# Kernel tuning notes

Measured on AMD Instinct MI355X. Metric: run time of the kernel, lower is better.

## Reference

```python
import jax, jax.numpy as jnp
import numpy as np

B, T, V, D, C, O = 64, 128, 32, 128, 10000, 512


def setup_inputs() -> dict:
    key = jax.random.key(0)
    ks = jax.random.split(key, 14)
    s = 1.0 / np.sqrt(D)
    # ragged visit sequences: codes in [1, C), padded visits are all-zero codes
    codes = jax.random.randint(ks[0], (B, T, V), 1, C, dtype=jnp.int32)
    lengths = jax.random.randint(ks[1], (B,), 1, T + 1, dtype=jnp.int32)
    visit_mask = (jnp.arange(T)[None, :] < lengths[:, None])
    codes_x = codes * visit_mask[:, :, None].astype(jnp.int32)
    emb = (jax.random.normal(ks[2], (C, D), jnp.float32) * 0.02).at[0].set(0.0)
    return {
        "codes_x": codes_x,
        "emb": emb,
        "a_kernel": jax.random.normal(ks[3], (D, 3 * D), jnp.float32) * s,
        "a_rec": jax.random.normal(ks[4], (D, 3 * D), jnp.float32) * s,
        "a_bias": jnp.zeros((2, 3 * D), jnp.float32),
        "b_kernel": jax.random.normal(ks[5], (D, 3 * D), jnp.float32) * s,
        "b_rec": jax.random.normal(ks[6], (D, 3 * D), jnp.float32) * s,
        "b_bias": jnp.zeros((2, 3 * D), jnp.float32),
        "alpha_w": jax.random.normal(ks[7], (D, 1), jnp.float32) * s,
        "alpha_b": jnp.zeros((1,), jnp.float32),
        "beta_w": jax.random.normal(ks[8], (D, D), jnp.float32) * s,
        "beta_b": jnp.zeros((D,), jnp.float32),
        "cls_w": jax.random.normal(ks[9], (D, O), jnp.float32) * s,
        "cls_b": jnp.zeros((O,), jnp.float32),
    }


def gru(x, mask, kernel, rec, bias):
    """Keras GRU (reset_after=True), masked: carries state+output through padded steps.
    x: [B,T,D], mask: [B,T] bool -> [B,T,D]."""
    bi, br = bias[0], bias[1]
    xp = x @ kernel + bi  # [B,T,3D] precomputed input projection

    def step(h, inp):
        xp_t, m_t = inp
        hp = h @ rec + br
        xz, xr, xh = jnp.split(xp_t, 3, axis=-1)
        hz, hr, hh = jnp.split(hp, 3, axis=-1)
        z = jax.nn.sigmoid(xz + hz)
        r = jax.nn.sigmoid(xr + hr)
        hcand = jnp.tanh(xh + r * hh)
        h_new = z * h + (1.0 - z) * hcand
        h_out = jnp.where(m_t[:, None], h_new, h)
        return h_out, h_out

    h0 = jnp.zeros((x.shape[0], rec.shape[0]), x.dtype)
    _, ys = jax.lax.scan(step, h0, (jnp.swapaxes(xp, 0, 1), jnp.swapaxes(mask, 0, 1)))
    return jnp.swapaxes(ys, 0, 1)


def retain_forward(codes_x, emb, a_kernel, a_rec, a_bias, b_kernel, b_rec, b_bias,
                   alpha_w, alpha_b, beta_w, beta_b, cls_w, cls_b):
    x = emb[codes_x].sum(axis=2)                     # [B,T,D] visit embeddings
    mask = x.sum(axis=-1) != 0                       # [B,T] visit mask
    lengths = mask.sum(axis=-1)                      # [B]
    # masked reverse: rx[b, j] = x[b, lengths[b]-1-j] for j < lengths[b], else 0
    t = x.shape[1]
    idx = lengths[:, None] - 1 - jnp.arange(t)[None, :]  # [B,T]
    valid = idx >= 0
    rx = jnp.take_along_axis(x, jnp.clip(idx, 0, t - 1)[:, :, None], axis=1)
    rx = rx * valid[:, :, None].astype(x.dtype)
    # dual GRU attention (dropout inactive at inference)
    g = gru(rx, mask, a_kernel, a_rec, a_bias)
    h = gru(rx, mask, b_kernel, b_rec, b_bias)
    attn_alpha = jax.nn.softmax(g @ alpha_w + alpha_b, axis=1)   # [B,T,1]
    attn_beta = jnp.tanh(h @ beta_w + beta_b)                    # [B,T,D]
    c = jnp.sum(attn_alpha * attn_beta * x, axis=1)              # [B,D]
    return c @ cls_w + cls_b                                     # [B,O]


def reference(codes_x, emb, a_kernel, a_rec, a_bias, b_kernel, b_rec, b_bias,
              alpha_w, alpha_b, beta_w, beta_b, cls_w, cls_b):
    return retain_forward(codes_x, emb, a_kernel, a_rec, a_bias, b_kernel, b_rec,
                          b_bias, alpha_w, alpha_b, beta_w, beta_b, cls_w, cls_b)
```

## Files before the change

kernel.cpp:

```cpp
#include <hip/hip_runtime.h>
#include <math.h>

#define BATCH 64
#define TT 128
#define VV 32
#define DD 128
#define OO 512
#define N3 384
#define NN 768

#define OFF_X      0u
#define OFF_XPC    1048576u
#define OFF_GSEQ   7340032u
#define OFF_HSEQ   8388608u
#define OFF_INTS   9437184u
#define OFF_ALPHA  9453632u
#define OFF_CPART  9461824u

__global__ __launch_bounds__(128) void k_gather(const int* __restrict__ codes,
        const float* __restrict__ emb, float* __restrict__ x, int* __restrict__ mask) {
    int bt = blockIdx.x;
    int d = threadIdx.x;
    const int* cp = codes + (size_t)bt * VV;
    float acc = 0.f;
    #pragma unroll 8
    for (int v = 0; v < VV; ++v) {
        int code = cp[v];
        acc += emb[(size_t)code * DD + d];
    }
    x[(size_t)bt * DD + d] = acc;
    float s = acc;
    #pragma unroll
    for (int off = 32; off; off >>= 1) s += __shfl_xor(s, off);
    __shared__ float red[2];
    if ((d & 63) == 0) red[d >> 6] = s;
    __syncthreads();
    if (d == 0) mask[bt] = ((red[0] + red[1]) != 0.0f) ? 1 : 0;
}

__global__ __launch_bounds__(128) void k_len(const int* __restrict__ mask,
        int* __restrict__ lengths, int* __restrict__ ridx) {
    int b = blockIdx.x, t = threadIdx.x;
    int m = mask[b * TT + t];
    unsigned long long bal = __ballot(m != 0);
    __shared__ int cnt[2];
    if ((t & 63) == 0) cnt[t >> 6] = __popcll(bal);
    __syncthreads();
    int len = cnt[0] + cnt[1];
    if (t == 0) lengths[b] = len;
    ridx[b * TT + t] = len - 1 - t;
}

__global__ __launch_bounds__(256) void k_xp(const float* __restrict__ x,
        const float* __restrict__ akern, const float* __restrict__ bkern,
        const float* __restrict__ abias, const float* __restrict__ bbias,
        float* __restrict__ xpc) {
    __shared__ __attribute__((aligned(16))) float As[32][68];
    __shared__ __attribute__((aligned(16))) float Bs[32][68];
    int mb = blockIdx.x, nb = blockIdx.y;
    int n0 = nb * 64;
    int tid = threadIdx.x;
    int tx = tid & 15, ty = tid >> 4;
    float acc[4][4] = {};
    for (int k0 = 0; k0 < DD; k0 += 32) {
        #pragma unroll
        for (int i = 0; i < 2; ++i) {
            int s = tid * 2 + i;
            int row = s >> 3, kk = (s & 7) * 4;
            float4 v = *reinterpret_cast<const float4*>(x + (size_t)(mb * 64 + row) * DD + k0 + kk);
            As[kk][row] = v.x; As[kk+1][row] = v.y; As[kk+2][row] = v.z; As[kk+3][row] = v.w;
        }
        #pragma unroll
        for (int i = 0; i < 2; ++i) {
            int s = tid * 2 + i;
            int kk = s >> 4, c = (s & 15) * 4;
            int n = n0 + c;
            const float* src = (n < N3) ? (akern + (size_t)(k0 + kk) * N3 + n)
                                        : (bkern + (size_t)(k0 + kk) * N3 + (n - N3));
            *reinterpret_cast<float4*>(&Bs[kk][c]) = *reinterpret_cast<const float4*>(src);
        }
        __syncthreads();
        #pragma unroll
        for (int kk = 0; kk < 32; ++kk) {
            float4 a = *reinterpret_cast<const float4*>(&As[kk][ty * 4]);
            float4 bv = *reinterpret_cast<const float4*>(&Bs[kk][tx * 4]);
            float av[4] = {a.x, a.y, a.z, a.w};
            float bw[4] = {bv.x, bv.y, bv.z, bv.w};
            #pragma unroll
            for (int i2 = 0; i2 < 4; ++i2)
                #pragma unroll
                for (int j2 = 0; j2 < 4; ++j2)
                    acc[i2][j2] = fmaf(av[i2], bw[j2], acc[i2][j2]);
        }
        __syncthreads();
    }
    int nbase = n0 + tx * 4;
    float4 bias;
    if (nbase < N3) bias = *reinterpret_cast<const float4*>(abias + nbase);
    else            bias = *reinterpret_cast<const float4*>(bbias + (nbase - N3));
    #pragma unroll
    for (int i2 = 0; i2 < 4; ++i2) {
        int m = mb * 64 + ty * 4 + i2;
        float4 o;
        o.x = acc[i2][0] + bias.x; o.y = acc[i2][1] + bias.y;
        o.z = acc[i2][2] + bias.z; o.w = acc[i2][3] + bias.w;
        *reinterpret_cast<float4*>(xpc + (size_t)m * NN + nbase) = o;
    }
}

__device__ __forceinline__ float fast_sigmoid(float x) {
    return 1.f / (1.f + __expf(-x));
}
__device__ __forceinline__ float fast_tanh(float x) {
    float xc = fminf(fmaxf(x, -15.f), 15.f);
    float e2 = __expf(2.f * xc);
    return (e2 - 1.f) / (e2 + 1.f);
}

#define LOADW(i) \
    float4 w##i = *reinterpret_cast<const float4*>(rec + (size_t)(krow0 + i) * N3 + j4); \
    asm volatile("" : "+v"(w##i.x), "+v"(w##i.y), "+v"(w##i.z), "+v"(w##i.w));
#define DOTQ(q, i0, i1, i2, i3) { \
    float4 hv = *reinterpret_cast<const float4*>(&h_lds[krow0 + 4 * (q)]); \
    acc.x = fmaf(hv.x, w##i0.x, acc.x); acc.y = fmaf(hv.x, w##i0.y, acc.y); \
    acc.z = fmaf(hv.x, w##i0.z, acc.z); acc.w = fmaf(hv.x, w##i0.w, acc.w); \
    acc.x = fmaf(hv.y, w##i1.x, acc.x); acc.y = fmaf(hv.y, w##i1.y, acc.y); \
    acc.z = fmaf(hv.y, w##i1.z, acc.z); acc.w = fmaf(hv.y, w##i1.w, acc.w); \
    acc.x = fmaf(hv.z, w##i2.x, acc.x); acc.y = fmaf(hv.z, w##i2.y, acc.y); \
    acc.z = fmaf(hv.z, w##i2.z, acc.z); acc.w = fmaf(hv.z, w##i2.w, acc.w); \
    acc.x = fmaf(hv.w, w##i3.x, acc.x); acc.y = fmaf(hv.w, w##i3.y, acc.y); \
    acc.z = fmaf(hv.w, w##i3.z, acc.z); acc.w = fmaf(hv.w, w##i3.w, acc.w); }

__global__ __launch_bounds__(768, 3)
void k_gru(
        const float* __restrict__ arec, const float* __restrict__ abias,
        const float* __restrict__ brec, const float* __restrict__ bbias,
        const float* __restrict__ xpc, const int* __restrict__ mask,
        const int* __restrict__ ridx, float* __restrict__ gseq, float* __restrict__ hseq) {
    int b = blockIdx.x & 63;
    int gru = blockIdx.x >> 6;
    const float* rec  = gru ? brec : arec;
    const float* bias = gru ? bbias : abias;
    float* seq = gru ? hseq : gseq;
    int t = threadIdx.x;
    int c4 = t % 96;
    int kc = t / 96;
    int j4 = c4 * 4;
    int krow0 = kc * 16;
    LOADW(0)  LOADW(1)  LOADW(2)  LOADW(3)
    LOADW(4)  LOADW(5)  LOADW(6)  LOADW(7)
    LOADW(8)  LOADW(9)  LOADW(10) LOADW(11)
    LOADW(12) LOADW(13) LOADW(14) LOADW(15)
    __shared__ __attribute__((aligned(16))) float h_lds[DD];
    __shared__ __attribute__((aligned(16))) float part[8 * N3];
    __shared__ int smask[TT];
    __shared__ int sridx[TT];
    if (t < TT) { smask[t] = mask[b * TT + t]; sridx[t] = ridx[b * TT + t]; }
    if (t < DD) h_lds[t] = 0.f;
    float bz_r = 0.f, br_r = 0.f, bh_r = 0.f, bz_i = 0.f, br_i = 0.f, bh_i = 0.f;
    if (t < DD) {
        bz_r = bias[N3 + t];  br_r = bias[N3 + DD + t];  bh_r = bias[N3 + 2 * DD + t];
        bz_i = bias[t];       br_i = bias[DD + t];       bh_i = bias[2 * DD + t];
    }
    float hreg = 0.f;
    __syncthreads();
    const float* xpb = xpc + (size_t)b * TT * NN + gru * N3;
    for (int step = 0; step < TT; ++step) {
        int m = smask[step];
        if (!m) {
            if (t < DD) seq[(size_t)(b * TT + step) * DD + t] = hreg;
            continue;
        }
        float xz = 0.f, xr = 0.f, xh = 0.f;
        if (t < DD) {
            int row = sridx[step];
            if (row >= 0) {
                const float* xrow = xpb + (size_t)row * NN;
                xz = xrow[t]; xr = xrow[DD + t]; xh = xrow[2 * DD + t];
            } else {
                xz = bz_i; xr = br_i; xh = bh_i;
            }
        }
        float4 acc = {0.f, 0.f, 0.f, 0.f};
        DOTQ(0, 0, 1, 2, 3)
        DOTQ(1, 4, 5, 6, 7)
        DOTQ(2, 8, 9, 10, 11)
        DOTQ(3, 12, 13, 14, 15)
        *reinterpret_cast<float4*>(&part[kc * N3 + j4]) = acc;
        __syncthreads();
        if (t < DD) {
            float hz = bz_r, hr = br_r, hh = bh_r;
            #pragma unroll
            for (int g = 0; g < 8; ++g) {
                hz += part[g * N3 + t];
                hr += part[g * N3 + DD + t];
                hh += part[g * N3 + 2 * DD + t];
            }
            float z = fast_sigmoid(xz + hz);
            float r = fast_sigmoid(xr + hr);
            float hc = fast_tanh(xh + r * hh);
            float hnew = z * hreg + (1.f - z) * hc;
            hreg = hnew;
            h_lds[t] = hnew;
            seq[(size_t)(b * TT + step) * DD + t] = hnew;
        }
        __syncthreads();
    }
}

__global__ __launch_bounds__(128) void k_alpha(const float* __restrict__ gseq,
        const float* __restrict__ alpha_w, const float* __restrict__ alpha_b,
        float* __restrict__ alpha) {
    int b = blockIdx.x, t = threadIdx.x;
    __shared__ float aw[DD];
    aw[t] = alpha_w[t];
    __syncthreads();
    const float* g = gseq + (size_t)(b * TT + t) * DD;
    float acc = 0.f;
    #pragma unroll
    for (int k = 0; k < DD; k += 4) {
        float4 gv = *reinterpret_cast<const float4*>(g + k);
        acc = fmaf(gv.x, aw[k],     acc);
        acc = fmaf(gv.y, aw[k + 1], acc);
        acc = fmaf(gv.z, aw[k + 2], acc);
        acc = fmaf(gv.w, aw[k + 3], acc);
    }
    float logit = acc + alpha_b[0];
    float mx = logit;
    #pragma unroll
    for (int off = 32; off; off >>= 1) mx = fmaxf(mx, __shfl_xor(mx, off));
    __shared__ float redm[2];
    if ((t & 63) == 0) redm[t >> 6] = mx;
    __syncthreads();
    mx = fmaxf(redm[0], redm[1]);
    float e = expf(logit - mx);
    float s = e;
    #pragma unroll
    for (int off = 32; off; off >>= 1) s += __shfl_xor(s, off);
    __shared__ float reds[2];
    if ((t & 63) == 0) reds[t >> 6] = s;
    __syncthreads();
    alpha[b * TT + t] = e / (reds[0] + reds[1]);
}

__global__ __launch_bounds__(128) void k_beta(const float* __restrict__ hseq,
        const float* __restrict__ x, const float* __restrict__ beta_w,
        const float* __restrict__ beta_b, const float* __restrict__ alpha,
        float* __restrict__ cpart) {
    __shared__ __attribute__((aligned(16))) float bw[DD][DD];
    __shared__ __attribute__((aligned(16))) float hr[4][DD];
    __shared__ float cred[4][DD];
    int b = blockIdx.x >> 3, grp = blockIdx.x & 7;
    int tid = threadIdx.x;
    for (int i = tid; i < DD * DD / 4; i += 128) {
        float4 v = *reinterpret_cast<const float4*>(beta_w + (size_t)i * 4);
        *reinterpret_cast<float4*>(&bw[0][0] + (size_t)i * 4) = v;
    }
    int trow = tid >> 5, dq = (tid & 31) * 4;
    float bb0 = beta_b[dq], bb1 = beta_b[dq + 1], bb2 = beta_b[dq + 2], bb3 = beta_b[dq + 3];
    float c0 = 0.f, c1 = 0.f, c2 = 0.f, c3 = 0.f;
    for (int tg = 0; tg < 4; ++tg) {
        int t = grp * 16 + tg * 4 + trow;
        size_t rowoff = (size_t)(b * TT + t) * DD;
        float4 hv = *reinterpret_cast<const float4*>(hseq + rowoff + dq);
        __syncthreads();
        *reinterpret_cast<float4*>(&hr[trow][dq]) = hv;
        __syncthreads();
        float a0 = 0.f, a1 = 0.f, a2 = 0.f, a3 = 0.f;
        #pragma unroll 8
        for (int k = 0; k < DD; ++k) {
            float hk = hr[trow][k];
            float4 w = *reinterpret_cast<const float4*>(&bw[k][dq]);
            a0 = fmaf(hk, w.x, a0); a1 = fmaf(hk, w.y, a1);
            a2 = fmaf(hk, w.z, a2); a3 = fmaf(hk, w.w, a3);
        }
        float al = alpha[b * TT + t];
        float4 xv = *reinterpret_cast<const float4*>(x + rowoff + dq);
        c0 = fmaf(al * tanhf(a0 + bb0), xv.x, c0);
        c1 = fmaf(al * tanhf(a1 + bb1), xv.y, c1);
        c2 = fmaf(al * tanhf(a2 + bb2), xv.z, c2);
        c3 = fmaf(al * tanhf(a3 + bb3), xv.w, c3);
    }
    cred[trow][dq] = c0; cred[trow][dq + 1] = c1;
    cred[trow][dq + 2] = c2; cred[trow][dq + 3] = c3;
    __syncthreads();
    if (tid < 32) {
        #pragma unroll
        for (int i = 0; i < 4; ++i) {
            int d = tid * 4 + i;
            float sum = cred[0][d] + cred[1][d] + cred[2][d] + cred[3][d];
            cpart[(size_t)(b * 8 + grp) * DD + d] = sum;
        }
    }
}

__global__ __launch_bounds__(256) void k_out(const float* __restrict__ cpart,
        const float* __restrict__ cls_w, const float* __restrict__ cls_b,
        float* __restrict__ out) {
    __shared__ float cl[DD];
    int b = blockIdx.x, tid = threadIdx.x;
    if (tid < DD) {
        float s = 0.f;
        #pragma unroll
        for (int p = 0; p < 8; ++p) s += cpart[(size_t)(b * 8 + p) * DD + tid];
        cl[tid] = s;
    }
    __syncthreads();
    #pragma unroll
    for (int rep = 0; rep < 2; ++rep) {
        int o = tid + rep * 256;
        float acc = cls_b[o];
        #pragma unroll 8
        for (int k = 0; k < DD; ++k)
            acc = fmaf(cl[k], cls_w[(size_t)k * OO + o], acc);
        out[(size_t)b * OO + o] = acc;
    }
}

extern "C" void kernel_launch(void* const* d_in, const int* in_sizes, int n_in,
                              void* d_out, int out_size, void* d_ws, size_t ws_size,
                              hipStream_t stream) {
    const int*   codes   = (const int*)d_in[0];
    const float* emb     = (const float*)d_in[1];
    const float* akern   = (const float*)d_in[2];
    const float* arec    = (const float*)d_in[3];
    const float* abias   = (const float*)d_in[4];
    const float* bkern   = (const float*)d_in[5];
    const float* brec    = (const float*)d_in[6];
    const float* bbias   = (const float*)d_in[7];
    const float* alpha_w = (const float*)d_in[8];
    const float* alpha_b = (const float*)d_in[9];
    const float* beta_w  = (const float*)d_in[10];
    const float* beta_b  = (const float*)d_in[11];
    const float* cls_w   = (const float*)d_in[12];
    const float* cls_b   = (const float*)d_in[13];
    float* ws   = (float*)d_ws;
    float* x    = ws + OFF_X;
    float* xpc  = ws + OFF_XPC;
    float* gseq = ws + OFF_GSEQ;
    float* hseq = ws + OFF_HSEQ;
    int*   ints = (int*)(ws + OFF_INTS);
    int* mask    = ints;
    int* ridx    = ints + 8192;
    int* lengths = ints + 16384;
    float* alpha = ws + OFF_ALPHA;
    float* cpart = ws + OFF_CPART;
    float* out   = (float*)d_out;

    k_gather<<<BATCH * TT, 128, 0, stream>>>(codes, emb, x, mask);
    k_len<<<BATCH, 128, 0, stream>>>(mask, lengths, ridx);
    dim3 g3(128, 12);
    k_xp<<<g3, 256, 0, stream>>>(x, akern, bkern, abias, bbias, xpc);
    k_gru<<<128, 768, 0, stream>>>(arec, abias, brec, bbias, xpc, mask, ridx, gseq, hseq);
    k_alpha<<<BATCH, 128, 0, stream>>>(gseq, alpha_w, alpha_b, alpha);
    k_beta<<<BATCH * 8, 128, 0, stream>>>(hseq, x, beta_w, beta_b, alpha, cpart);
    k_out<<<BATCH, 256, 0, stream>>>(cpart, cls_w, cls_b, out);
}
```

Baseline: 170.7 us.

## Fuse length calc into GRU, fuse alpha softmax into beta, truncate GRU loop

```diff
diff --git a/kernel.cpp b/kernel.cpp
--- a/kernel.cpp
+++ b/kernel.cpp
@@ -14,7 +14,6 @@
 #define OFF_GSEQ   7340032u
 #define OFF_HSEQ   8388608u
 #define OFF_INTS   9437184u
-#define OFF_ALPHA  9453632u
 #define OFF_CPART  9461824u
 
 __global__ __launch_bounds__(128) void k_gather(const int* __restrict__ codes,
@@ -36,19 +35,6 @@
     if ((d & 63) == 0) red[d >> 6] = s;
     __syncthreads();
     if (d == 0) mask[bt] = ((red[0] + red[1]) != 0.0f) ? 1 : 0;
-}
-
-__global__ __launch_bounds__(128) void k_len(const int* __restrict__ mask,
-        int* __restrict__ lengths, int* __restrict__ ridx) {
-    int b = blockIdx.x, t = threadIdx.x;
-    int m = mask[b * TT + t];
-    unsigned long long bal = __ballot(m != 0);
-    __shared__ int cnt[2];
-    if ((t & 63) == 0) cnt[t >> 6] = __popcll(bal);
-    __syncthreads();
-    int len = cnt[0] + cnt[1];
-    if (t == 0) lengths[b] = len;
-    ridx[b * TT + t] = len - 1 - t;
 }
 
 __global__ __launch_bounds__(256) void k_xp(const float* __restrict__ x,
@@ -136,7 +122,7 @@
         const float* __restrict__ arec, const float* __restrict__ abias,
         const float* __restrict__ brec, const float* __restrict__ bbias,
         const float* __restrict__ xpc, const int* __restrict__ mask,
-        const int* __restrict__ ridx, float* __restrict__ gseq, float* __restrict__ hseq) {
+        float* __restrict__ gseq, float* __restrict__ hseq) {
     int b = blockIdx.x & 63;
     int gru = blockIdx.x >> 6;
     const float* rec  = gru ? brec : arec;
@@ -155,7 +141,17 @@
     __shared__ __attribute__((aligned(16))) float part[8 * N3];
     __shared__ int smask[TT];
     __shared__ int sridx[TT];
-    if (t < TT) { smask[t] = mask[b * TT + t]; sridx[t] = ridx[b * TT + t]; }
+    __shared__ int scnt[2];
+    __shared__ int shi[2];
+    if (t < 2 * 64) {
+        int m = mask[b * TT + t];
+        smask[t] = m;
+        unsigned long long bal = __ballot(m != 0);
+        if ((t & 63) == 0) {
+            scnt[t >> 6] = __popcll(bal);
+            shi[t >> 6] = bal ? (63 - __clzll(bal)) : -1;
+        }
+    }
     if (t < DD) h_lds[t] = 0.f;
     float bz_r = 0.f, br_r = 0.f, bh_r = 0.f, bz_i = 0.f, br_i = 0.f, bh_i = 0.f;
     if (t < DD) {
@@ -164,8 +160,12 @@
     }
     float hreg = 0.f;
     __syncthreads();
+    int len  = scnt[0] + scnt[1];
+    int last = (shi[1] >= 0) ? (64 + shi[1]) : shi[0];
+    if (t < TT) sridx[t] = len - 1 - t;
+    __syncthreads();
     const float* xpb = xpc + (size_t)b * TT * NN + gru * N3;
-    for (int step = 0; step < TT; ++step) {
+    for (int step = 0; step <= last; ++step) {
         int m = smask[step];
         if (!m) {
             if (t < DD) seq[(size_t)(b * TT + step) * DD + t] = hreg;
@@ -206,55 +206,56 @@
         }
         __syncthreads();
     }
-}
-
-__global__ __launch_bounds__(128) void k_alpha(const float* __restrict__ gseq,
+    if (t < DD) {
+        for (int step = last + 1; step < TT; ++step)
+            seq[(size_t)(b * TT + step) * DD + t] = hreg;
+    }
+}
+
+__global__ __launch_bounds__(128) void k_ab(const float* __restrict__ gseq,
         const float* __restrict__ alpha_w, const float* __restrict__ alpha_b,
-        float* __restrict__ alpha) {
-    int b = blockIdx.x, t = threadIdx.x;
-    __shared__ float aw[DD];
-    aw[t] = alpha_w[t];
-    __syncthreads();
-    const float* g = gseq + (size_t)(b * TT + t) * DD;
-    float acc = 0.f;
-    #pragma unroll
-    for (int k = 0; k < DD; k += 4) {
-        float4 gv = *reinterpret_cast<const float4*>(g + k);
-        acc = fmaf(gv.x, aw[k],     acc);
-        acc = fmaf(gv.y, aw[k + 1], acc);
-        acc = fmaf(gv.z, aw[k + 2], acc);
-        acc = fmaf(gv.w, aw[k + 3], acc);
-    }
-    float logit = acc + alpha_b[0];
-    float mx = logit;
-    #pragma unroll
-    for (int off = 32; off; off >>= 1) mx = fmaxf(mx, __shfl_xor(mx, off));
-    __shared__ float redm[2];
-    if ((t & 63) == 0) redm[t >> 6] = mx;
-    __syncthreads();
-    mx = fmaxf(redm[0], redm[1]);
-    float e = expf(logit - mx);
-    float s = e;
-    #pragma unroll
-    for (int off = 32; off; off >>= 1) s += __shfl_xor(s, off);
-    __shared__ float reds[2];
-    if ((t & 63) == 0) reds[t >> 6] = s;
-    __syncthreads();
-    alpha[b * TT + t] = e / (reds[0] + reds[1]);
-}
-
-__global__ __launch_bounds__(128) void k_beta(const float* __restrict__ hseq,
-        const float* __restrict__ x, const float* __restrict__ beta_w,
-        const float* __restrict__ beta_b, const float* __restrict__ alpha,
+        const float* __restrict__ hseq, const float* __restrict__ x,
+        const float* __restrict__ beta_w, const float* __restrict__ beta_b,
         float* __restrict__ cpart) {
     __shared__ __attribute__((aligned(16))) float bw[DD][DD];
     __shared__ __attribute__((aligned(16))) float hr[4][DD];
     __shared__ float cred[4][DD];
+    __shared__ float aw[DD];
+    __shared__ float salpha[TT];
+    __shared__ float redm[2], reds[2];
     int b = blockIdx.x >> 3, grp = blockIdx.x & 7;
     int tid = threadIdx.x;
     for (int i = tid; i < DD * DD / 4; i += 128) {
         float4 v = *reinterpret_cast<const float4*>(beta_w + (size_t)i * 4);
         *reinterpret_cast<float4*>(&bw[0][0] + (size_t)i * 4) = v;
+    }
+    aw[tid] = alpha_w[tid];
+    __syncthreads();
+    {
+        const float* g = gseq + (size_t)(b * TT + tid) * DD;
+        float acc = 0.f;
+        #pragma unroll
+        for (int k = 0; k < DD; k += 4) {
+            float4 gv = *reinterpret_cast<const float4*>(g + k);
+            acc = fmaf(gv.x, aw[k],     acc);
+            acc = fmaf(gv.y, aw[k + 1], acc);
+            acc = fmaf(gv.z, aw[k + 2], acc);
+            acc = fmaf(gv.w, aw[k + 3], acc);
+        }
+        float logit = acc + alpha_b[0];
+        float mx = logit;
+        #pragma unroll
+        for (int off = 32; off; off >>= 1) mx = fmaxf(mx, __shfl_xor(mx, off));
+        if ((tid & 63) == 0) redm[tid >> 6] = mx;
+        __syncthreads();
+        mx = fmaxf(redm[0], redm[1]);
+        float e = expf(logit - mx);
+        float s = e;
+        #pragma unroll
+        for (int off = 32; off; off >>= 1) s += __shfl_xor(s, off);
+        if ((tid & 63) == 0) reds[tid >> 6] = s;
+        __syncthreads();
+        salpha[tid] = e / (reds[0] + reds[1]);
     }
     int trow = tid >> 5, dq = (tid & 31) * 4;
     float bb0 = beta_b[dq], bb1 = beta_b[dq + 1], bb2 = beta_b[dq + 2], bb3 = beta_b[dq + 3];
@@ -274,7 +275,7 @@
             a0 = fmaf(hk, w.x, a0); a1 = fmaf(hk, w.y, a1);
             a2 = fmaf(hk, w.z, a2); a3 = fmaf(hk, w.w, a3);
         }
-        float al = alpha[b * TT + t];
+        float al = salpha[t];
         float4 xv = *reinterpret_cast<const float4*>(x + rowoff + dq);
         c0 = fmaf(al * tanhf(a0 + bb0), xv.x, c0);
         c1 = fmaf(al * tanhf(a1 + bb1), xv.y, c1);
@@ -339,20 +340,14 @@
     float* xpc  = ws + OFF_XPC;
     float* gseq = ws + OFF_GSEQ;
     float* hseq = ws + OFF_HSEQ;
-    int*   ints = (int*)(ws + OFF_INTS);
-    int* mask    = ints;
-    int* ridx    = ints + 8192;
-    int* lengths = ints + 16384;
-    float* alpha = ws + OFF_ALPHA;
+    int*   mask = (int*)(ws + OFF_INTS);
     float* cpart = ws + OFF_CPART;
     float* out   = (float*)d_out;
 
     k_gather<<<BATCH * TT, 128, 0, stream>>>(codes, emb, x, mask);
-    k_len<<<BATCH, 128, 0, stream>>>(mask, lengths, ridx);
     dim3 g3(128, 12);
     k_xp<<<g3, 256, 0, stream>>>(x, akern, bkern, abias, bbias, xpc);
-    k_gru<<<128, 768, 0, stream>>>(arec, abias, brec, bbias, xpc, mask, ridx, gseq, hseq);
-    k_alpha<<<BATCH, 128, 0, stream>>>(gseq, alpha_w, alpha_b, alpha);
-    k_beta<<<BATCH * 8, 128, 0, stream>>>(hseq, x, beta_w, beta_b, alpha, cpart);
+    k_gru<<<128, 768, 0, stream>>>(arec, abias, brec, bbias, xpc, mask, gseq, hseq);
+    k_ab<<<BATCH * 8, 128, 0, stream>>>(gseq, alpha_w, alpha_b, hseq, x, beta_w, beta_b, cpart);
     k_out<<<BATCH, 256, 0, stream>>>(cpart, cls_w, cls_b, out);
 }
```

Result: no change. 172.7 us (+1.1%).
